# Optimization experiments

Hardware: AMD Instinct MI355X
Metric: run time of the kernel (lower is better)

## Reference

```python
import jax, jax.numpy as jnp
import numpy as np

N_NODES = 100000
N_EDGES = 800000
F_IN = 128
F_OUT = 128
K_HOPS = 2


def setup_inputs() -> dict:
    key = jax.random.key(0)
    k1, k2, k3 = jax.random.split(key, 3)
    x = jax.random.normal(k1, (N_NODES, F_IN), dtype=jnp.float32)
    edge_index = jax.random.randint(k2, (2, N_EDGES), 0, N_NODES, dtype=jnp.int64)
    # SGConv's internal Linear(num_features -> embedding_size), bias=True
    W = jax.random.normal(k3, (F_OUT, F_IN), dtype=jnp.float32) * (1.0 / np.sqrt(F_IN))
    b = jnp.zeros((F_OUT,), dtype=jnp.float32)
    return {"x": x, "W": W, "b": b, "edge_index": edge_index}


def reference(x, W, b, edge_index):
    N = x.shape[0]
    # gcn_norm: add self loops (weight 1), symmetric normalization D^-1/2 (A+I) D^-1/2
    loop = jnp.arange(N, dtype=edge_index.dtype)
    row = jnp.concatenate([edge_index[0], loop])  # source nodes j
    col = jnp.concatenate([edge_index[1], loop])  # target nodes i
    ones = jnp.ones(row.shape[0], dtype=x.dtype)
    deg = jax.ops.segment_sum(ones, col, num_segments=N)
    dinv = jnp.where(deg > 0, jax.lax.rsqrt(deg), jnp.zeros_like(deg))
    norm = dinv[row] * dinv[col]  # [E+N]
    # K-hop propagation: x <- segment_sum(norm * x[row] -> col)
    h = x
    for _ in range(K_HOPS):
        h = jax.ops.segment_sum(norm[:, None] * h[row], col, num_segments=N)
    out = h @ W.T + b  # [N, F_OUT]
    return jax.nn.log_softmax(out, axis=1)
```

## Files before the change

kernel.cpp:

```cpp
#include <hip/hip_runtime.h>
#include <math.h>

#define N_NODES 100000
#define N_EDGES 800000
#define F 128
#define NBUCK ((N_NODES + 255) / 256)
#define NREP 8
#define SCAP_R 512
#define CPAD 32
#define BSPAN 4096

typedef __attribute__((ext_vector_type(8))) short short8;
typedef __attribute__((ext_vector_type(4))) float floatx4;

__device__ __forceinline__ unsigned short f2bf(float f) {
    unsigned u = __float_as_uint(f);
    u += 0x7fffu + ((u >> 16) & 1u);
    return (unsigned short)(u >> 16);
}
__device__ __forceinline__ float bf_lo(unsigned u) { return __uint_as_float(u << 16); }
__device__ __forceinline__ float bf_hi(unsigned u) { return __uint_as_float(u & 0xffff0000u); }
__device__ __forceinline__ unsigned pack2(float a, float b) {
    return (unsigned)f2bf(a) | ((unsigned)f2bf(b) << 16);
}


__global__ void k_fill2(const int* __restrict__ row, const int* __restrict__ col,
                        int* __restrict__ bcnt, unsigned* __restrict__ stage) {
    int e = blockIdx.x * blockDim.x + threadIdx.x;
    if (e >= N_EDGES) return;
    int r = row[e], c = col[e];
    int bk = c >> 8;
    int ctr = (bk << 3) | (blockIdx.x & (NREP - 1));
    int p = atomicAdd(&bcnt[ctr * CPAD], 1);
    if (p < SCAP_R)
        stage[(size_t)ctr * SCAP_R + p] = ((unsigned)(c & 255) << 20) | (unsigned)(r + 1);
}


__global__ __launch_bounds__(256) void k_build(const int* __restrict__ bcnt,
                                               const unsigned* __restrict__ stage,
                                               unsigned* __restrict__ csr,
                                               int2* __restrict__ rp2,
                                               float* __restrict__ dinv,
                                               float* __restrict__ dinv2) {
    __shared__ int hist[256];
    __shared__ int sc[256];
    __shared__ int cursor[256];
    __shared__ int spanTot;
    __shared__ unsigned img[BSPAN];
    int bk = blockIdx.x, t = threadIdx.x;
    hist[t] = 0;
    __syncthreads();
#pragma unroll
    for (int rep = 0; rep < NREP; ++rep) {
        int ctr = (bk << 3) | rep;
        int n = bcnt[ctr * CPAD]; n = n < SCAP_R ? n : SCAP_R;
        const unsigned* sp = stage + (size_t)ctr * SCAP_R;
        for (int i = t; i < n; i += 256) atomicAdd(&hist[sp[i] >> 20], 1);
    }
    __syncthreads();
    int cdeg = hist[t];
    int pad = (cdeg + 7) & ~7;
    sc[t] = pad;
    __syncthreads();
#pragma unroll
    for (int off = 1; off < 256; off <<= 1) {
        int u = (t >= off) ? sc[t - off] : 0;
        __syncthreads();
        sc[t] += u;
        __syncthreads();
    }
    int excl = sc[t] - pad;
    if (t == 255) spanTot = sc[255];
    cursor[t] = excl;
    __syncthreads();
    int tot = spanTot;
    int node = bk * 256 + t;
    if (node < N_NODES) {
        int base = bk * BSPAN;
        rp2[node] = (int2){base + excl, base + excl + pad};
        float d = rsqrtf((float)cdeg + 1.0f);
        dinv[node] = d; dinv2[node] = d * d;
    }
    for (int i = t; i < tot; i += 256) img[i] = 0u;
    __syncthreads();
#pragma unroll
    for (int rep = 0; rep < NREP; ++rep) {
        int ctr = (bk << 3) | rep;
        int n = bcnt[ctr * CPAD]; n = n < SCAP_R ? n : SCAP_R;
        const unsigned* sp = stage + (size_t)ctr * SCAP_R;
        for (int i = t; i < n; i += 256) {
            unsigned v = sp[i];
            int pos = atomicAdd(&cursor[v >> 20], 1);
            img[pos] = v & 0xFFFFFu;
        }
    }
    __syncthreads();
    unsigned* op = csr + (size_t)bk * BSPAN;
    for (int i = t; i < tot; i += 256) op[i] = img[i];
}

__global__ void k_prep(const float4* __restrict__ x, const float* __restrict__ dinv,
                       const float4* __restrict__ W4, uint2* __restrict__ wbf,
                       uint2* __restrict__ xb, uint2* __restrict__ h1b) {
    int i = blockIdx.x * blockDim.x + threadIdx.x;
    if (i < 32) { xb[i] = (uint2){0u, 0u}; h1b[i] = (uint2){0u, 0u}; }
    if (i < 4096) {
        float4 wv = W4[i];
        uint2 o; o.x = pack2(wv.x, wv.y); o.y = pack2(wv.z, wv.w);
        wbf[i] = o;
    }
    if (i >= N_NODES * 32) return;
    int node = i >> 5;
    float d = dinv[node];
    float4 v = x[i];
    uint2 o; o.x = pack2(d * v.x, d * v.y); o.y = pack2(d * v.z, d * v.w);
    xb[i + 32] = o;
}


__global__ __launch_bounds__(256) void k_hop(const int2* __restrict__ rp2,
                                             const unsigned* __restrict__ csr,
                                             const float* __restrict__ scale,
                                             const uint2* __restrict__ src,
                                             uint2* __restrict__ dst) {
    int wv = (blockIdx.x * blockDim.x + threadIdx.x) >> 6;
    int lane = threadIdx.x & 63;
    int half = lane >> 5, off = lane & 31;
    int node = wv * 2 + half;
    if (node >= N_NODES) return;
    uint2 u = src[(size_t)(node + 1) * 32 + off];
    float a0 = bf_lo(u.x), a1 = bf_hi(u.x);
    float a2 = bf_lo(u.y), a3 = bf_hi(u.y);
    int2 rp = rp2[node];
    int e = rp.x, end = rp.y;
    for (; e < end; e += 8) {
        const uint4* cp = (const uint4*)(csr + e);
        uint4 c0 = cp[0], c1 = cp[1];
        unsigned idx[8] = {c0.x, c0.y, c0.z, c0.w, c1.x, c1.y, c1.z, c1.w};
#pragma unroll
        for (int j = 0; j < 8; ++j) {
            uint2 v = src[(size_t)idx[j] * 32 + off];
            a0 += bf_lo(v.x); a1 += bf_hi(v.x);
            a2 += bf_lo(v.y); a3 += bf_hi(v.y);
        }
    }
    float s = scale[node];
    uint2 o; o.x = pack2(s * a0, s * a1); o.y = pack2(s * a2, s * a3);
    dst[(size_t)(node + 1) * 32 + off] = o;
}


__global__ __launch_bounds__(256) void k_gemm_lsm_mfma(const unsigned short* __restrict__ h,
                                                       const unsigned short* __restrict__ wbf,
                                                       const float* __restrict__ b,
                                                       float* __restrict__ out) {
    int tid = threadIdx.x;
    int lane = tid & 63;
    int wave = tid >> 6;
    int m = lane & 15, quad = lane >> 4;

    float bv[8];
#pragma unroll
    for (int t = 0; t < 8; ++t) bv[t] = b[16 * t + m];

    const int ngroups = (N_NODES + 63) / 64;
    for (int g = blockIdx.x; g < ngroups; g += gridDim.x) {
        int gbase = g * 64 + wave * 16;
        int nodeA = gbase + m;
        int node_c = nodeA < N_NODES ? nodeA : N_NODES - 1;
        short8 a[4];
#pragma unroll
        for (int ks = 0; ks < 4; ++ks)
            a[ks] = *(const short8*)(h + (size_t)node_c * 128 + ks * 32 + quad * 8);
        floatx4 acc[8];
#pragma unroll
        for (int t = 0; t < 8; ++t) acc[t] = (floatx4){bv[t], bv[t], bv[t], bv[t]};
#pragma unroll
        for (int t = 0; t < 8; ++t) {
#pragma unroll
            for (int ks = 0; ks < 4; ++ks) {
                short8 bf = *(const short8*)(wbf + (size_t)(16 * t + m) * 128 + ks * 32 + quad * 8);
                acc[t] = __builtin_amdgcn_mfma_f32_16x16x32_bf16(a[ks], bf, acc[t], 0, 0, 0);
            }
        }

#pragma unroll
        for (int r = 0; r < 4; ++r) {
            float mx = acc[0][r];
#pragma unroll
            for (int t = 1; t < 8; ++t) mx = fmaxf(mx, acc[t][r]);
#pragma unroll
            for (int msk = 1; msk < 16; msk <<= 1) mx = fmaxf(mx, __shfl_xor(mx, msk));
            float sm = 0.f;
#pragma unroll
            for (int t = 0; t < 8; ++t) sm += __expf(acc[t][r] - mx);
#pragma unroll
            for (int msk = 1; msk < 16; msk <<= 1) sm += __shfl_xor(sm, msk);
            float l = mx + __logf(sm);
            int rown = gbase + quad * 4 + r;
            if (rown < N_NODES) {
                float* op = out + (size_t)rown * 128 + m;
#pragma unroll
                for (int t = 0; t < 8; ++t) op[16 * t] = acc[t][r] - l;
            }
        }
    }
}


extern "C" void kernel_launch(void* const* d_in, const int* in_sizes, int n_in,
                              void* d_out, int out_size, void* d_ws, size_t ws_size,
                              hipStream_t stream) {
    const float* x = (const float*)d_in[0];
    const float* W = (const float*)d_in[1];
    const float* b = (const float*)d_in[2];
    const int* edge = (const int*)d_in[3];
    const int* row = edge;
    const int* col = edge + N_EDGES;
    float* out = (float*)d_out;

    int*      bcnt  = (int*)d_ws;
    float*    dinv  = (float*)(bcnt + NBUCK * NREP * CPAD + 256);
    float*    dinv2 = dinv + 102400;
    int2*     rp2   = (int2*)(dinv2 + 102400);
    unsigned* csr   = (unsigned*)(rp2 + 102400);
    uint2*    xb    = (uint2*)(csr + (size_t)NBUCK * BSPAN);
    uint2*    h1b   = xb + 32 * (N_NODES + 1);
    uint2*    h2b   = xb;
    unsigned* stage = (unsigned*)(h1b + 32);
    uint2*    wbf   = h1b + 32 * (N_NODES + 1);

    int nb_edges = (N_EDGES + 255) / 256;
    int nb_prep = (N_NODES * 32 + 255) / 256;

    (void)hipMemsetAsync(bcnt, 0, (size_t)NBUCK * NREP * CPAD * 4, stream);
    k_fill2<<<nb_edges, 256, 0, stream>>>(row, col, bcnt, stage);
    k_build<<<NBUCK, 256, 0, stream>>>(bcnt, stage, csr, rp2, dinv, dinv2);
    k_prep<<<nb_prep, 256, 0, stream>>>((const float4*)x, dinv, (const float4*)W, wbf, xb, h1b);

    int hop_blocks = (N_NODES / 2 * 64) / 256;
    k_hop<<<hop_blocks, 256, 0, stream>>>(rp2, csr, dinv2, xb, h1b);
    k_hop<<<hop_blocks, 256, 0, stream>>>(rp2, csr, dinv, h1b, h2b);

    k_gemm_lsm_mfma<<<512, 256, 0, stream>>>((const unsigned short*)(h2b + 32),
                                             (const unsigned short*)wbf, b, out);
}
```

Baseline: 245.5 us.

## Aggregate edge bucketing in shared memory before global atomic reservation

```diff
diff --git a/kernel.cpp b/kernel.cpp
--- a/kernel.cpp
+++ b/kernel.cpp
@@ -5,10 +5,11 @@
 #define N_EDGES 800000
 #define F 128
 #define NBUCK ((N_NODES + 255) / 256)
-#define NREP 8
-#define SCAP_R 512
 #define CPAD 32
+#define SCAP 3072
 #define BSPAN 4096
+#define EPB 2048
+#define FILL_BLOCKS ((N_EDGES + EPB - 1) / EPB)
 
 typedef __attribute__((ext_vector_type(8))) short short8;
 typedef __attribute__((ext_vector_type(4))) float floatx4;
@@ -25,16 +26,81 @@
 }
 
 
-__global__ void k_fill2(const int* __restrict__ row, const int* __restrict__ col,
-                        int* __restrict__ bcnt, unsigned* __restrict__ stage) {
-    int e = blockIdx.x * blockDim.x + threadIdx.x;
-    if (e >= N_EDGES) return;
-    int r = row[e], c = col[e];
-    int bk = c >> 8;
-    int ctr = (bk << 3) | (blockIdx.x & (NREP - 1));
-    int p = atomicAdd(&bcnt[ctr * CPAD], 1);
-    if (p < SCAP_R)
-        stage[(size_t)ctr * SCAP_R + p] = ((unsigned)(c & 255) << 20) | (unsigned)(r + 1);
+__global__ __launch_bounds__(256) void k_fill3(const int* __restrict__ row,
+                                               const int* __restrict__ col,
+                                               int* __restrict__ bcnt,
+                                               unsigned* __restrict__ stage) {
+    __shared__ int hist[512];
+    __shared__ int base[512];
+    __shared__ int gpos[NBUCK];
+    __shared__ int sA[256], sB[256];
+    __shared__ unsigned buf[EPB];
+    __shared__ unsigned short bkt[EPB];
+    int t = threadIdx.x, blk = blockIdx.x;
+    int e0 = blk * EPB;
+    int nedge = N_EDGES - e0; if (nedge > EPB) nedge = EPB;
+
+    hist[t] = 0; hist[256 + t] = 0;
+    __syncthreads();
+
+    int myb[8]; unsigned myv[8];
+#pragma unroll
+    for (int k = 0; k < 8; ++k) {
+        int i = t + k * 256;
+        myb[k] = -1;
+        if (i < nedge) {
+            int e = e0 + i;
+            int r = row[e], c = col[e];
+            int bk = c >> 8;
+            myb[k] = bk;
+            myv[k] = ((unsigned)(c & 255) << 20) | (unsigned)(r + 1);
+            atomicAdd(&hist[bk], 1);
+        }
+    }
+    __syncthreads();
+
+    int v0 = hist[t], v1 = hist[256 + t];
+    sA[t] = v0; __syncthreads();
+#pragma unroll
+    for (int off = 1; off < 256; off <<= 1) {
+        int u = (t >= off) ? sA[t - off] : 0;
+        __syncthreads(); sA[t] += u; __syncthreads();
+    }
+    int tot0 = sA[255];
+    sB[t] = v1; __syncthreads();
+#pragma unroll
+    for (int off = 1; off < 256; off <<= 1) {
+        int u = (t >= off) ? sB[t - off] : 0;
+        __syncthreads(); sB[t] += u; __syncthreads();
+    }
+    base[t] = sA[t] - v0;
+    base[256 + t] = tot0 + sB[t] - v1;
+    __syncthreads();
+    hist[t] = base[t]; hist[256 + t] = base[256 + t];
+    __syncthreads();
+
+#pragma unroll
+    for (int k = 0; k < 8; ++k) {
+        if (myb[k] >= 0) {
+            int pos = atomicAdd(&hist[myb[k]], 1);
+            buf[pos] = myv[k];
+            bkt[pos] = (unsigned short)myb[k];
+        }
+    }
+    __syncthreads();
+
+    for (int i = t; i < NBUCK; i += 256) {
+        int cnt = hist[i] - base[i];
+        gpos[i] = cnt > 0 ? atomicAdd(&bcnt[i * CPAD], cnt) : 0;
+    }
+    __syncthreads();
+
+    for (int i = t; i < nedge; i += 256) {
+        int bk = bkt[i];
+        int op = gpos[bk] + (i - base[bk]);
+        if (op < SCAP)
+            stage[(size_t)bk * SCAP + op] = buf[i];
+    }
 }
 
 
@@ -50,15 +116,11 @@
     __shared__ int spanTot;
     __shared__ unsigned img[BSPAN];
     int bk = blockIdx.x, t = threadIdx.x;
+    int n = bcnt[bk * CPAD]; n = n < SCAP ? n : SCAP;
+    const unsigned* sp = stage + (size_t)bk * SCAP;
     hist[t] = 0;
     __syncthreads();
-#pragma unroll
-    for (int rep = 0; rep < NREP; ++rep) {
-        int ctr = (bk << 3) | rep;
-        int n = bcnt[ctr * CPAD]; n = n < SCAP_R ? n : SCAP_R;
-        const unsigned* sp = stage + (size_t)ctr * SCAP_R;
-        for (int i = t; i < n; i += 256) atomicAdd(&hist[sp[i] >> 20], 1);
-    }
+    for (int i = t; i < n; i += 256) atomicAdd(&hist[sp[i] >> 20], 1);
     __syncthreads();
     int cdeg = hist[t];
     int pad = (cdeg + 7) & ~7;
@@ -85,16 +147,10 @@
     }
     for (int i = t; i < tot; i += 256) img[i] = 0u;
     __syncthreads();
-#pragma unroll
-    for (int rep = 0; rep < NREP; ++rep) {
-        int ctr = (bk << 3) | rep;
-        int n = bcnt[ctr * CPAD]; n = n < SCAP_R ? n : SCAP_R;
-        const unsigned* sp = stage + (size_t)ctr * SCAP_R;
-        for (int i = t; i < n; i += 256) {
-            unsigned v = sp[i];
-            int pos = atomicAdd(&cursor[v >> 20], 1);
-            img[pos] = v & 0xFFFFFu;
-        }
+    for (int i = t; i < n; i += 256) {
+        unsigned v = sp[i];
+        int pos = atomicAdd(&cursor[v >> 20], 1);
+        img[pos] = v & 0xFFFFFu;
     }
     __syncthreads();
     unsigned* op = csr + (size_t)bk * BSPAN;
@@ -222,7 +278,7 @@
     float* out = (float*)d_out;
 
     int*      bcnt  = (int*)d_ws;
-    float*    dinv  = (float*)(bcnt + NBUCK * NREP * CPAD + 256);
+    float*    dinv  = (float*)(bcnt + NBUCK * CPAD + 256);
     float*    dinv2 = dinv + 102400;
     int2*     rp2   = (int2*)(dinv2 + 102400);
     unsigned* csr   = (unsigned*)(rp2 + 102400);
@@ -232,11 +288,10 @@
     unsigned* stage = (unsigned*)(h1b + 32);
     uint2*    wbf   = h1b + 32 * (N_NODES + 1);
 
-    int nb_edges = (N_EDGES + 255) / 256;
     int nb_prep = (N_NODES * 32 + 255) / 256;
 
-    (void)hipMemsetAsync(bcnt, 0, (size_t)NBUCK * NREP * CPAD * 4, stream);
-    k_fill2<<<nb_edges, 256, 0, stream>>>(row, col, bcnt, stage);
+    (void)hipMemsetAsync(bcnt, 0, (size_t)NBUCK * CPAD * 4, stream);
+    k_fill3<<<FILL_BLOCKS, 256, 0, stream>>>(row, col, bcnt, stage);
     k_build<<<NBUCK, 256, 0, stream>>>(bcnt, stage, csr, rp2, dinv, dinv2);
     k_prep<<<nb_prep, 256, 0, stream>>>((const float4*)x, dinv, (const float4*)W, wbf, xb, h1b);
 
```

New measurement: 219.1 us. -10.7%, faster.
